# Kernel optimization log

Hardware: AMD Instinct MI355X
Metric: run time of the kernel (lower is better)

Reference implementation:

```python
import jax, jax.numpy as jnp
import numpy as np

EMSIZE = 2048
NCLASS = 128
D1 = 2
D2 = 2
NSENT = 32768


def setup_inputs() -> dict:
    key = jax.random.key(0)
    k1, k2, k3 = jax.random.split(key, 3)
    x = jax.random.normal(k1, (NSENT, 1, EMSIZE), dtype=jnp.float32)
    # Scaled-normal params (original uses nn.init.normal_; scaling keeps tanh unsaturated)
    W1 = jax.random.normal(k2, (D1 + 1, EMSIZE, NCLASS), dtype=jnp.float32) / np.float32(np.sqrt(EMSIZE))
    b1 = jnp.zeros((1, NCLASS), dtype=jnp.float32)
    W2 = jax.random.normal(k3, (D2 + 1, NCLASS, NCLASS), dtype=jnp.float32) / np.float32(np.sqrt(NCLASS))
    b2 = jnp.zeros((1, NCLASS), dtype=jnp.float32)
    return {"structural_representations": x, "W1": W1, "b1": b1, "W2": W2, "b2": b2}


def _shift_down(y, k, n):
    # y[p] -> y[p-k], zeros for p < k (causal shift along sentence axis)
    return jnp.pad(y, ((k, 0), (0, 0)))[:n] if k > 0 else y


def reference(structural_representations, W1, b1, W2, b2):
    x = structural_representations  # [N, 1, E]
    n, _, e = x.shape
    d1 = W1.shape[0] - 1
    d2 = W2.shape[0] - 1
    c = W1.shape[-1]
    xs = x.reshape(n, e)  # [N, E]

    # Stage 1: S[p] = sum_{k=0..d1, k<=p} (x[p-k] @ W1[k] + b1)
    Y = jnp.einsum('ne,kec->knc', xs, W1)  # [d1+1, N, C]: one big GEMM per tap
    S = sum(_shift_down(Y[k], k, n) for k in range(d1 + 1))  # windowed causal sum
    pos = jnp.arange(n)
    cnt1 = (jnp.minimum(pos, d1) + 1).astype(xs.dtype)  # bias added once per valid tap
    H = jnp.tanh(S + cnt1[:, None] * b1[0])  # [N, C]

    # Stage 2 (i >= d2): Z[i] = sum_{j=0..d2} H[i-d2+j] @ W2[j] + (d2+1)*b2
    G = jnp.einsum('nc,kcd->knd', H, W2)  # [d2+1, N, C]
    Z = sum(_shift_down(G[j], d2 - j, n) for j in range(d2 + 1)) + (d2 + 1) * b2[0]

    # Fallback for i < d2: single term tanh(x[i]@W1[0]+b1) @ W2[0] + b2
    H0 = jnp.tanh(xs @ W1[0] + b1[0])
    Z0 = H0 @ W2[0] + b2[0]
    Z = jnp.where((pos >= d2)[:, None], Z, Z0)

    out = jax.nn.log_softmax(Z, axis=-1)
    return out.reshape(n, 1, c)
```

## Files before the change

### kernel.cpp

```cpp
#include <hip/hip_runtime.h>
#include <math.h>

typedef __attribute__((ext_vector_type(8))) short short8;
typedef __attribute__((ext_vector_type(4))) float f32x4;

#define MFMA16(a, b, c) __builtin_amdgcn_mfma_f32_16x16x32_bf16((a), (b), (c), 0, 0, 0)

__device__ inline void gl_lds16(const void* g, void* l) {
  __builtin_amdgcn_global_load_lds(
      (const __attribute__((address_space(1))) void*)g,
      (__attribute__((address_space(3))) void*)l, 16, 0, 0);
}

__device__ inline unsigned int pack2(float lo, float hi) {
  unsigned int ulo = __float_as_uint(lo), uhi = __float_as_uint(hi);
  return (uhi & 0xFFFF0000u) | (ulo >> 16);
}
__device__ inline unsigned short f2bf_r(float f) {
  return (unsigned short)((__float_as_uint(f) + 0x8000u) >> 16);
}
__device__ inline float bf2f(unsigned short h) {
  return __uint_as_float(((unsigned int)h) << 16);
}

__global__ __launch_bounds__(256) void k_repack(const float* __restrict__ W1,
                                                const float* __restrict__ W2,
                                                unsigned short* __restrict__ W1bt,
                                                unsigned short* __restrict__ W2t) {
  __shared__ float tile[64 * 128];
  const int b = blockIdx.x, tid = threadIdx.x;
  if (b < 96) {
    const int k = b >> 5, et = b & 31;
    const int e0 = et * 64;
    const float* src = W1 + (size_t)k * 262144 + (size_t)e0 * 128;
#pragma unroll
    for (int i = 0; i < 8; ++i) {
      int idx4 = tid + i * 256;
      ((f32x4*)tile)[idx4] = ((const f32x4*)src)[idx4];
    }
    __syncthreads();
#pragma unroll
    for (int i = 0; i < 4; ++i) {
      int item = tid + i * 256;
      int c = item >> 3, eo = (item & 7) * 8;
      union { unsigned short h[8]; uint4 v; } t;
#pragma unroll
      for (int u = 0; u < 8; ++u) t.h[u] = f2bf_r(tile[(eo + u) * 128 + c]);
      *(uint4*)(W1bt + (size_t)(k * 128 + c) * 2048 + e0 + eo) = t.v;
    }
  } else {
    int idx = (b - 96) * 256 + tid;
    int j = idx >> 14, r = idx & 16383, d = r >> 7, c = r & 127;
    W2t[idx] = f2bf_r(W2[(size_t)j * 16384 + (size_t)c * 128 + d]);
  }
}

__global__ __launch_bounds__(256, 2) void k_fused(const float* __restrict__ X,
                                                  const unsigned short* __restrict__ Bt,
                                                  const unsigned short* __restrict__ W2t,
                                                  const float* __restrict__ b1,
                                                  const float* __restrict__ b2,
                                                  float* __restrict__ out) {
  __shared__ __align__(16) char smem[67584];
  unsigned short* Yt = (unsigned short*)smem;
  float* zbuf = (float*)(smem + 62720);

  const int r0 = blockIdx.x * 64;
  const int tid = threadIdx.x, wave = tid >> 6, lane = tid & 63;
  const int mrow = lane & 15, quad = lane >> 4;

  const float* agp[3];
  {
    const int aj[3] = { wave, wave + 4, 8 };
#pragma unroll
    for (int jj = 0; jj < 3; ++jj) {
      int j = aj[jj];
      int g = r0 - 4 + j * 8 + (lane >> 3);
      if (g < 0) g = 0;
      if (g > 32767) g = 32767;
      int c = (lane & 7) ^ (lane >> 3);
      agp[jj] = X + (size_t)g * 2048 + c * 4;
    }
  }
  const unsigned short* bgp[6];
#pragma unroll
  for (int jj = 0; jj < 6; ++jj) {
    int col = wave * 96 + jj * 16 + (lane >> 2);
    int c = (lane & 3) ^ ((lane >> 2) & 3);
    bgp[jj] = Bt + (size_t)col * 2048 + c * 8;
  }

  f32x4 acc[5][6] = {};

  auto stage = [&](char* base) {
    char* An = base;
    char* Bn = base + 9216;
    gl_lds16(agp[0], An + wave * 1024);
    gl_lds16(agp[1], An + (wave + 4) * 1024);
    if (wave == 0) gl_lds16(agp[2], An + 8 * 1024);
#pragma unroll
    for (int jj = 0; jj < 6; ++jj)
      gl_lds16(bgp[jj], Bn + (wave * 6 + jj) * 1024);
#pragma unroll
    for (int jj = 0; jj < 3; ++jj) agp[jj] += 32;
#pragma unroll
    for (int jj = 0; jj < 6; ++jj) bgp[jj] += 32;
  };

  stage(smem);
  __syncthreads();

#pragma unroll 2
  for (int t = 0; t < 64; ++t) {
    const int cur = t & 1;
    if (t < 63) stage(smem + (cur ^ 1) * 33792);

    const float* Af = (const float*)(smem + cur * 33792);
    const unsigned short* Bh = (const unsigned short*)(smem + cur * 33792 + 9216);

    short8 af[5];
#pragma unroll
    for (int rt = 0; rt < 5; ++rt) {
      int row = rt * 16 + mrow;
      int c0 = quad * 2;
      const float* base = Af + row * 32;
      f32x4 x0 = *(const f32x4*)(base + ((c0 ^ (mrow & 7)) * 4));
      f32x4 x1 = *(const f32x4*)(base + (((c0 + 1) ^ (mrow & 7)) * 4));
      union { unsigned int u[4]; short8 v; } tt;
      tt.u[0] = pack2(x0[0], x0[1]); tt.u[1] = pack2(x0[2], x0[3]);
      tt.u[2] = pack2(x1[0], x1[1]); tt.u[3] = pack2(x1[2], x1[3]);
      af[rt] = tt.v;
    }
#pragma unroll
    for (int ct = 0; ct < 6; ++ct) {
      int col = wave * 96 + ct * 16 + mrow;
      int sl = quad ^ (mrow & 3);
      short8 bf = *(const short8*)(Bh + col * 32 + sl * 8);
#pragma unroll
      for (int rt = 0; rt < 5; ++rt)
        acc[rt][ct] = MFMA16(af[rt], bf, acc[rt][ct]);
    }
    __syncthreads();
  }

#pragma unroll
  for (int rt = 0; rt < 5; ++rt)
#pragma unroll
    for (int ct = 0; ct < 6; ++ct)
#pragma unroll
      for (int rg = 0; rg < 4; ++rg) {
        int l = rt * 16 + quad * 4 + rg;
        int col = wave * 96 + ct * 16 + mrow;
        Yt[l * 392 + col] = f2bf_r(acc[rt][ct][rg]);
      }
  __syncthreads();

  for (int idx = tid; idx < 66 * 128; idx += 256) {
    int hl = idx >> 7, c = idx & 127;
    int p = r0 - 2 + hl;
    int i = hl + 2;
    float h = 0.f;
    if (p >= 0) {
      float s = bf2f(Yt[i * 392 + c]);
      float cnt = 1.f;
      if (p >= 1) { s += bf2f(Yt[(i - 1) * 392 + 128 + c]); cnt += 1.f; }
      if (p >= 2) { s += bf2f(Yt[(i - 2) * 392 + 256 + c]); cnt += 1.f; }
      h = tanhf(fmaf(cnt, b1[c], s));
    }
    Yt[(i - 2) * 392 + 256 + c] = f2bf_r(h);
  }
  __syncthreads();

  f32x4 acc2[8] = {};
#pragma unroll
  for (int j = 0; j < 3; ++j) {
#pragma unroll
    for (int kk = 0; kk < 4; ++kk) {
      short8 a0 = *(const short8*)&Yt[(wave * 16 + mrow + j) * 392 + 256 + kk * 32 + quad * 8];
      const unsigned short* wp = W2t + (size_t)(j * 128 + mrow) * 128 + kk * 32 + quad * 8;
#pragma unroll
      for (int ct = 0; ct < 8; ++ct)
        acc2[ct] = MFMA16(a0, *(const short8*)(wp + ct * 16 * 128), acc2[ct]);
    }
  }

#pragma unroll
  for (int rg = 0; rg < 4; ++rg) {
    float z[8]; float m = -1e30f;
#pragma unroll
    for (int ct = 0; ct < 8; ++ct) {
      z[ct] = acc2[ct][rg] + 3.f * b2[ct * 16 + mrow];
      m = fmaxf(m, z[ct]);
    }
#pragma unroll
    for (int off = 1; off < 16; off <<= 1) m = fmaxf(m, __shfl_xor(m, off, 64));
    float s = 0.f;
#pragma unroll
    for (int ct = 0; ct < 8; ++ct) s += __expf(z[ct] - m);
#pragma unroll
    for (int off = 1; off < 16; off <<= 1) s += __shfl_xor(s, off, 64);
    float lse = m + __logf(s);
    int grow = r0 + wave * 16 + quad * 4 + rg;
    if (grow >= 2) {
      float* op = out + (size_t)grow * 128 + mrow;
#pragma unroll
      for (int ct = 0; ct < 8; ++ct) op[ct * 16] = z[ct] - lse;
    }
  }

  if (blockIdx.x == 0) {
    __syncthreads();
    int row = tid >> 7, d = tid & 127;
    zbuf[row * 128 + d] = tanhf(bf2f(Yt[(row + 4) * 392 + d]) + b1[d]);
    __syncthreads();
    float zv = b2[d];
    for (int c = 0; c < 128; ++c)
      zv = fmaf(zbuf[row * 128 + c], bf2f(W2t[(size_t)d * 128 + c]), zv);
    __syncthreads();
    zbuf[row * 128 + d] = zv;
    __syncthreads();
    float m = -1e30f;
    for (int c = 0; c < 128; ++c) m = fmaxf(m, zbuf[row * 128 + c]);
    float s = 0.f;
    for (int c = 0; c < 128; ++c) s += __expf(zbuf[row * 128 + c] - m);
    out[(size_t)row * 128 + d] = zv - m - __logf(s);
  }
}

extern "C" void kernel_launch(void* const* d_in, const int* in_sizes, int n_in,
                              void* d_out, int out_size, void* d_ws, size_t ws_size,
                              hipStream_t stream) {
  const float* X  = (const float*)d_in[0];
  const float* W1 = (const float*)d_in[1];
  const float* b1 = (const float*)d_in[2];
  const float* W2 = (const float*)d_in[3];
  const float* b2 = (const float*)d_in[4];
  float* out = (float*)d_out;

  unsigned short* W1bt = (unsigned short*)d_ws;
  unsigned short* W2t  = (unsigned short*)((char*)d_ws + 1572864);

  k_repack<<<288, 256, 0, stream>>>(W1, W2, W1bt, W2t);
  k_fused<<<512, 256, 0, stream>>>(X, W1bt, W2t, b1, b2, out);
}
```

Baseline: 441.8 us.

## Use 128-row blocks with 512 threads and a triple-buffered async load pipeline

Each block now covers 128 output rows with 8 waves in a 2x4 wave grid instead of 64 rows with 4 waves. This cuts the halo overhead and the W1 tile reloads per output row. The K loop moves from double to triple buffering, using explicit vmcnt waits and raw s_barrier, so global-to-LDS loads run two stages ahead of the MFMA work. The A tile is stored in a plane-major layout and the B swizzle is changed. About 129KB of LDS allows only one block per CU, and the hand-tuned waitcnt counts depend on the exact number of loads per wave.

Result: no change. 441.6 us (-0.0%).

```diff
diff --git a/kernel.cpp b/kernel.cpp
--- a/kernel.cpp
+++ b/kernel.cpp
@@ -55,77 +55,68 @@
   }
 }
 
-__global__ __launch_bounds__(256, 2) void k_fused(const float* __restrict__ X,
+__global__ __launch_bounds__(512, 2) void k_fused(const float* __restrict__ X,
                                                   const unsigned short* __restrict__ Bt,
                                                   const unsigned short* __restrict__ W2t,
                                                   const float* __restrict__ b1,
                                                   const float* __restrict__ b2,
                                                   float* __restrict__ out) {
-  __shared__ __align__(16) char smem[67584];
+  constexpr int BUF = 43008, BOFF = 18432;
+  __shared__ __align__(16) char smem[3 * 43008];
   unsigned short* Yt = (unsigned short*)smem;
-  float* zbuf = (float*)(smem + 62720);
-
-  const int r0 = blockIdx.x * 64;
+  float* zbuf = (float*)(smem + 106624);
+
+  const int r0 = blockIdx.x * 128;
   const int tid = threadIdx.x, wave = tid >> 6, lane = tid & 63;
   const int mrow = lane & 15, quad = lane >> 4;
+  const int wr = wave >> 2, wc = wave & 3;
 
   const float* agp[3];
   {
-    const int aj[3] = { wave, wave + 4, 8 };
+    const int Ls[3] = { wave, wave + 8, 16 + wave };
 #pragma unroll
     for (int jj = 0; jj < 3; ++jj) {
-      int j = aj[jj];
-      int g = r0 - 4 + j * 8 + (lane >> 3);
+      int u = Ls[jj] * 64 + lane;
+      int pl = u / 144, rr = u - pl * 144;
+      if (pl > 7) pl = 7;
+      int g = r0 - 4 + rr;
       if (g < 0) g = 0;
       if (g > 32767) g = 32767;
-      int c = (lane & 7) ^ (lane >> 3);
-      agp[jj] = X + (size_t)g * 2048 + c * 4;
-    }
-  }
-  const unsigned short* bgp[6];
-#pragma unroll
-  for (int jj = 0; jj < 6; ++jj) {
-    int col = wave * 96 + jj * 16 + (lane >> 2);
-    int c = (lane & 3) ^ ((lane >> 2) & 3);
-    bgp[jj] = Bt + (size_t)col * 2048 + c * 8;
+      agp[jj] = X + (size_t)g * 2048 + pl * 4;
+    }
+  }
+  const unsigned short* bgp[3];
+#pragma unroll
+  for (int jj = 0; jj < 3; ++jj) {
+    int col = (wave * 3 + jj) * 16 + (lane >> 2);
+    int kc = (lane & 3) ^ ((lane >> 3) & 3);
+    bgp[jj] = Bt + (size_t)col * 2048 + kc * 8;
   }
 
   f32x4 acc[5][6] = {};
 
   auto stage = [&](char* base) {
-    char* An = base;
-    char* Bn = base + 9216;
-    gl_lds16(agp[0], An + wave * 1024);
-    gl_lds16(agp[1], An + (wave + 4) * 1024);
-    if (wave == 0) gl_lds16(agp[2], An + 8 * 1024);
-#pragma unroll
-    for (int jj = 0; jj < 6; ++jj)
-      gl_lds16(bgp[jj], Bn + (wave * 6 + jj) * 1024);
+    gl_lds16(agp[0], base + wave * 1024);
+    gl_lds16(agp[1], base + (wave + 8) * 1024);
+    if (wave < 2) gl_lds16(agp[2], base + (16 + wave) * 1024);
+#pragma unroll
+    for (int jj = 0; jj < 3; ++jj)
+      gl_lds16(bgp[jj], base + BOFF + (wave * 3 + jj) * 1024);
 #pragma unroll
     for (int jj = 0; jj < 3; ++jj) agp[jj] += 32;
 #pragma unroll
-    for (int jj = 0; jj < 6; ++jj) bgp[jj] += 32;
+    for (int jj = 0; jj < 3; ++jj) bgp[jj] += 32;
   };
 
-  stage(smem);
-  __syncthreads();
-
-#pragma unroll 2
-  for (int t = 0; t < 64; ++t) {
-    const int cur = t & 1;
-    if (t < 63) stage(smem + (cur ^ 1) * 33792);
-
-    const float* Af = (const float*)(smem + cur * 33792);
-    const unsigned short* Bh = (const unsigned short*)(smem + cur * 33792 + 9216);
-
+  auto compute = [&](const char* base) {
+    const char* Ab = base;
+    const unsigned short* Bb = (const unsigned short*)(base + BOFF);
     short8 af[5];
 #pragma unroll
     for (int rt = 0; rt < 5; ++rt) {
-      int row = rt * 16 + mrow;
-      int c0 = quad * 2;
-      const float* base = Af + row * 32;
-      f32x4 x0 = *(const f32x4*)(base + ((c0 ^ (mrow & 7)) * 4));
-      f32x4 x1 = *(const f32x4*)(base + (((c0 + 1) ^ (mrow & 7)) * 4));
+      int row = wr * 80 + rt * 16 + mrow;
+      f32x4 x0 = *(const f32x4*)(Ab + (quad * 2) * 2304 + row * 16);
+      f32x4 x1 = *(const f32x4*)(Ab + (quad * 2 + 1) * 2304 + row * 16);
       union { unsigned int u[4]; short8 v; } tt;
       tt.u[0] = pack2(x0[0], x0[1]); tt.u[1] = pack2(x0[2], x0[3]);
       tt.u[2] = pack2(x1[0], x1[1]); tt.u[3] = pack2(x1[2], x1[3]);
@@ -133,15 +124,34 @@
     }
 #pragma unroll
     for (int ct = 0; ct < 6; ++ct) {
-      int col = wave * 96 + ct * 16 + mrow;
-      int sl = quad ^ (mrow & 3);
-      short8 bf = *(const short8*)(Bh + col * 32 + sl * 8);
+      int col = wc * 96 + ct * 16 + mrow;
+      int slot = quad ^ ((mrow >> 1) & 3);
+      short8 bf = *(const short8*)(Bb + col * 32 + slot * 8);
 #pragma unroll
       for (int rt = 0; rt < 5; ++rt)
         acc[rt][ct] = MFMA16(af[rt], bf, acc[rt][ct]);
     }
-    __syncthreads();
-  }
+  };
+
+  stage(smem);
+  stage(smem + BUF);
+
+  int cur = 0, nx2 = 2;
+  for (int t = 0; t < 63; ++t) {
+    if (wave < 2) asm volatile("s_waitcnt vmcnt(6)" ::: "memory");
+    else          asm volatile("s_waitcnt vmcnt(5)" ::: "memory");
+    __builtin_amdgcn_s_barrier();
+    __builtin_amdgcn_sched_barrier(0);
+    if (t < 62) stage(smem + nx2 * BUF);
+    compute(smem + cur * BUF);
+    cur = (cur == 2) ? 0 : cur + 1;
+    nx2 = (nx2 == 2) ? 0 : nx2 + 1;
+  }
+  asm volatile("s_waitcnt vmcnt(0)" ::: "memory");
+  __builtin_amdgcn_s_barrier();
+  __builtin_amdgcn_sched_barrier(0);
+  compute(smem + cur * BUF);
+  __syncthreads();
 
 #pragma unroll
   for (int rt = 0; rt < 5; ++rt)
@@ -149,13 +159,13 @@
     for (int ct = 0; ct < 6; ++ct)
 #pragma unroll
       for (int rg = 0; rg < 4; ++rg) {
-        int l = rt * 16 + quad * 4 + rg;
-        int col = wave * 96 + ct * 16 + mrow;
-        Yt[l * 392 + col] = f2bf_r(acc[rt][ct][rg]);
+        int l = wr * 80 + rt * 16 + quad * 4 + rg;
+        int col = wc * 96 + ct * 16 + mrow;
+        if (l < 136) Yt[l * 392 + col] = f2bf_r(acc[rt][ct][rg]);
       }
   __syncthreads();
 
-  for (int idx = tid; idx < 66 * 128; idx += 256) {
+  for (int idx = tid; idx < 130 * 128; idx += 512) {
     int hl = idx >> 7, c = idx & 127;
     int p = r0 - 2 + hl;
     int i = hl + 2;
@@ -211,19 +221,25 @@
   if (blockIdx.x == 0) {
     __syncthreads();
     int row = tid >> 7, d = tid & 127;
-    zbuf[row * 128 + d] = tanhf(bf2f(Yt[(row + 4) * 392 + d]) + b1[d]);
-    __syncthreads();
-    float zv = b2[d];
-    for (int c = 0; c < 128; ++c)
-      zv = fmaf(zbuf[row * 128 + c], bf2f(W2t[(size_t)d * 128 + c]), zv);
-    __syncthreads();
-    zbuf[row * 128 + d] = zv;
-    __syncthreads();
-    float m = -1e30f;
-    for (int c = 0; c < 128; ++c) m = fmaxf(m, zbuf[row * 128 + c]);
-    float s = 0.f;
-    for (int c = 0; c < 128; ++c) s += __expf(zbuf[row * 128 + c] - m);
-    out[(size_t)row * 128 + d] = zv - m - __logf(s);
+    if (tid < 256)
+      zbuf[row * 128 + d] = tanhf(bf2f(Yt[(row + 4) * 392 + d]) + b1[d]);
+    __syncthreads();
+    float zv = 0.f;
+    if (tid < 256) {
+      zv = b2[d];
+      for (int c = 0; c < 128; ++c)
+        zv = fmaf(zbuf[row * 128 + c], bf2f(W2t[(size_t)d * 128 + c]), zv);
+    }
+    __syncthreads();
+    if (tid < 256) zbuf[row * 128 + d] = zv;
+    __syncthreads();
+    if (tid < 256) {
+      float m = -1e30f;
+      for (int c = 0; c < 128; ++c) m = fmaxf(m, zbuf[row * 128 + c]);
+      float s = 0.f;
+      for (int c = 0; c < 128; ++c) s += __expf(zbuf[row * 128 + c] - m);
+      out[(size_t)row * 128 + d] = zv - m - __logf(s);
+    }
   }
 }
 
@@ -241,5 +257,5 @@
   unsigned short* W2t  = (unsigned short*)((char*)d_ws + 1572864);
 
   k_repack<<<288, 256, 0, stream>>>(W1, W2, W1bt, W2t);
-  k_fused<<<512, 256, 0, stream>>>(X, W1bt, W2t, b1, b2, out);
-}
+  k_fused<<<256, 512, 0, stream>>>(X, W1bt, W2t, b1, b2, out);
+}
```
